# Kernel tuning notes

Hardware: AMD Instinct MI355X
Metric: run time of the kernel (lower is better)

## Reference

```python
import jax, jax.numpy as jnp
import numpy as np

N = 65536        # flattened ray-sample count
K = 8            # net_kernels (experts)
WID = 64         # net_width
D = 32           # feature dim (num_output_channels)
POS_DEG = 2
VIEW_DEG = 4
DIN = D + (3 + 2 * POS_DEG * 3) + (3 + 2 * VIEW_DEG * 3)  # 74


def posenc(x, deg):
    # coord.pos_enc with min_deg=0, max_deg=deg, append_identity=True
    scales = 2.0 ** jnp.arange(deg, dtype=x.dtype)            # [deg]
    xb = (x[..., None, :] * scales[:, None]).reshape(*x.shape[:-1], deg * x.shape[-1])
    four = jnp.sin(jnp.concatenate([xb, xb + 0.5 * jnp.pi], axis=-1))
    return jnp.concatenate([x, four], axis=-1)


def multi_dense(idx, x, kernel, bias):
    # per-sample expert gather + small matmul: x [N,din], kernel [K,din,dout]
    w = kernel[idx]                                           # [N,din,dout]
    return jnp.einsum('ni,nio->no', x, w) + bias[idx]


def _he_uniform(key, shape):
    fan_in = shape[-2]
    lim = np.sqrt(6.0 / fan_in).astype(np.float32)
    return jax.random.uniform(key, shape, jnp.float32, -lim, lim)


def setup_inputs() -> dict:
    key = jax.random.key(0)
    ks = jax.random.split(key, 8)
    idxs = jax.random.randint(ks[0], (N, 1), 0, K, dtype=jnp.int32)
    positions = jax.random.normal(ks[1], (N, 3), jnp.float32)
    viewdirs = jax.random.normal(ks[2], (N, 3), jnp.float32)
    viewdirs = viewdirs / jnp.linalg.norm(viewdirs, axis=-1, keepdims=True)
    features = jax.random.normal(ks[3], (N, D), jnp.float32)
    W0 = _he_uniform(ks[4], (K, DIN, WID))
    b0 = jnp.zeros((K, WID), jnp.float32)
    W1 = _he_uniform(ks[5], (K, WID, WID))
    b1 = jnp.zeros((K, WID), jnp.float32)
    W2 = _he_uniform(ks[6], (K, WID, D))
    b2 = jnp.zeros((K, D), jnp.float32)
    return {'idxs': idxs, 'positions': positions, 'viewdirs': viewdirs,
            'features': features, 'W0': W0, 'b0': b0, 'W1': W1, 'b1': b1,
            'W2': W2, 'b2': b2}


def reference(idxs, positions, viewdirs, features, W0, b0, W1, b1, W2, b2):
    idx = idxs.reshape(-1)                                    # [N]
    x = jnp.concatenate([features,
                         posenc(positions, POS_DEG),
                         posenc(viewdirs, VIEW_DEG)], axis=-1)  # [N, DIN]
    h = jax.nn.relu(multi_dense(idx, x, W0, b0))              # [N, WID]
    h = jax.nn.relu(multi_dense(idx, h, W1, b1))              # [N, WID]
    return multi_dense(idx, h, W2, b2)                        # [N, D]
```

## Files before the change

### kernel.cpp

```cpp
#include <hip/hip_runtime.h>
#include <hip/hip_bf16.h>

#define NS    65536
#define KEXP  8
#define WID   64
#define DOUT  32
#define DIN   74
#define TM    64
#define XS    104
#define HS    72
#define GX    64
#define NB    64

typedef __attribute__((ext_vector_type(8))) short short8;
typedef __attribute__((ext_vector_type(4))) float floatx4;

__device__ __forceinline__ unsigned short f2b(float f) {
  unsigned u = __builtin_bit_cast(unsigned, f);
  u = u + 0x7FFFu + ((u >> 16) & 1u);
  return (unsigned short)(u >> 16);
}


__global__ __launch_bounds__(1024) void k_scatter(const int* __restrict__ idxs,
                                                  unsigned short* __restrict__ bucket,
                                                  int* __restrict__ hist) {
  __shared__ int lc[KEXP];
  const int tid = threadIdx.x;
  const int b = blockIdx.x;
  if (tid < KEXP) lc[tid] = 0;
  __syncthreads();
  const int gid = b * 1024 + tid;
  const int e = idxs[gid];
  const int rank = atomicAdd(&lc[e], 1);
  bucket[(e << 16) + (b << 10) + rank] = (unsigned short)gid;
  __syncthreads();
  if (tid < KEXP) hist[b * KEXP + tid] = lc[tid];
}

__global__ __launch_bounds__(256) void k_mlp(
    const int* __restrict__ hist,
    const unsigned short* __restrict__ bucket,
    const float* __restrict__ pos,
    const float* __restrict__ view,
    const float* __restrict__ feat,
    const float* __restrict__ W0,
    const float* __restrict__ B0,
    const float* __restrict__ W1,
    const float* __restrict__ B1,
    const float* __restrict__ W2,
    const float* __restrict__ B2,
    float* __restrict__ out)
{
  const int e = blockIdx.y;
  const int tid = threadIdx.x;

  __shared__ __align__(16) unsigned short Xs[TM * XS];
  __shared__ __align__(16) unsigned short W0t[WID * XS];
  __shared__ __align__(16) unsigned short W1t[WID * HS];
  __shared__ __align__(16) unsigned short W2t[DOUT * HS];
  __shared__ __align__(16) unsigned short Hs[TM * HS];
  __shared__ float sb0[WID];
  __shared__ float sb1[WID];
  __shared__ float sb2[DOUT];
  __shared__ int sid[TM];
  __shared__ unsigned cns[NB];
  __shared__ unsigned pref[NB];

  if (tid < NB) {
    const unsigned c = (unsigned)hist[tid * KEXP + e];
    unsigned p = c;
    #pragma unroll
    for (int st = 1; st < NB; st <<= 1) {
      const unsigned v = __shfl_up(p, st, 64);
      if ((tid & 63) >= st) p += v;
    }
    cns[tid] = c;
    pref[tid] = p;
  }
  for (int i = tid; i < TM * XS; i += 256) Xs[i] = 0;
  for (int i = tid; i < WID * XS; i += 256) W0t[i] = 0;
  __syncthreads();

  const int segCnt = (int)pref[NB - 1];
  if ((int)blockIdx.x * TM >= segCnt) return;

  {
    const float* g0 = W0 + (size_t)e * DIN * WID;
    for (int g = tid; g < 19 * WID; g += 256) {
      const int o = g & 63, i4 = g >> 6, ib = i4 * 4;
      unsigned v0 = 0, v1 = 0;
      #pragma unroll
      for (int j = 0; j < 4; ++j) {
        const int i = ib + j;
        unsigned short w = (i < DIN) ? f2b(g0[i * WID + o]) : (unsigned short)0;
        if (j < 2) v0 |= (unsigned)w << (16 * j);
        else       v1 |= (unsigned)w << (16 * (j - 2));
      }
      *(uint2*)&W0t[o * XS + ib] = make_uint2(v0, v1);
    }
    const float* g1 = W1 + (size_t)e * WID * WID;
    for (int g = tid; g < 16 * WID; g += 256) {
      const int o = g & 63, i4 = g >> 6, ib = i4 * 4;
      unsigned v0, v1;
      v0 = (unsigned)f2b(g1[(ib + 0) * WID + o]) | ((unsigned)f2b(g1[(ib + 1) * WID + o]) << 16);
      v1 = (unsigned)f2b(g1[(ib + 2) * WID + o]) | ((unsigned)f2b(g1[(ib + 3) * WID + o]) << 16);
      *(uint2*)&W1t[o * HS + ib] = make_uint2(v0, v1);
    }
    const float* g2 = W2 + (size_t)e * WID * DOUT;
    for (int g = tid; g < 16 * DOUT; g += 256) {
      const int o = g & 31, i4 = g >> 5, ib = i4 * 4;
      unsigned v0, v1;
      v0 = (unsigned)f2b(g2[(ib + 0) * DOUT + o]) | ((unsigned)f2b(g2[(ib + 1) * DOUT + o]) << 16);
      v1 = (unsigned)f2b(g2[(ib + 2) * DOUT + o]) | ((unsigned)f2b(g2[(ib + 3) * DOUT + o]) << 16);
      *(uint2*)&W2t[o * HS + ib] = make_uint2(v0, v1);
    }
    if (tid < WID) {
      sb0[tid] = B0[e * WID + tid];
      sb1[tid] = B1[e * WID + tid];
    } else if (tid < WID + DOUT) {
      const int t = tid - WID;
      sb2[t] = B2[e * DOUT + t];
    }
  }
  __syncthreads();

  const int lane = tid & 63;
  const int wv = tid >> 6;
  const int quad = lane >> 4;
  const int r16 = lane & 15;
  const int rb = wv * 16;

  for (int tile = blockIdx.x; tile * TM < segCnt; tile += GX) {
    const int t0 = tile * TM;
    const int rows = min(TM, segCnt - t0);

    __syncthreads();

    const int r = lane;
    if (r < rows) {
      const int p = t0 + r;
      int lo = 0, hi = NB - 1;
      #pragma unroll
      for (int it = 0; it < 6; ++it) {
        const int mid = (lo + hi) >> 1;
        if (pref[mid] > (unsigned)p) hi = mid; else lo = mid + 1;
      }
      const int sb_ = lo;
      const int local = p - (int)(pref[sb_] - cns[sb_]);
      const int s = (int)bucket[(e << 16) + (sb_ << 10) + local];
      unsigned short* xr = &Xs[r * XS];
      if (wv == 0) {
        sid[r] = s;
        const float4* fs = (const float4*)(feat + (size_t)s * DOUT);
        #pragma unroll
        for (int q = 0; q < 4; ++q) {
          float4 f = fs[q];
          xr[q * 4 + 0] = f2b(f.x);
          xr[q * 4 + 1] = f2b(f.y);
          xr[q * 4 + 2] = f2b(f.z);
          xr[q * 4 + 3] = f2b(f.w);
        }
      } else if (wv == 1) {
        const float4* fs = (const float4*)(feat + (size_t)s * DOUT);
        #pragma unroll
        for (int q = 4; q < 8; ++q) {
          float4 f = fs[q];
          xr[q * 4 + 0] = f2b(f.x);
          xr[q * 4 + 1] = f2b(f.y);
          xr[q * 4 + 2] = f2b(f.z);
          xr[q * 4 + 3] = f2b(f.w);
        }
      } else if (wv == 2) {
        float p3[3];
        p3[0] = pos[s * 3 + 0];
        p3[1] = pos[s * 3 + 1];
        p3[2] = pos[s * 3 + 2];
        #pragma unroll
        for (int d = 0; d < 3; ++d) xr[32 + d] = f2b(p3[d]);
        #pragma unroll
        for (int si = 0; si < 2; ++si) {
          const float sc = (float)(1 << si);
          #pragma unroll
          for (int d = 0; d < 3; ++d) {
            const float a = p3[d] * sc;
            xr[35 + si * 3 + d] = f2b(__sinf(a));
            xr[41 + si * 3 + d] = f2b(__cosf(a));
          }
        }
      } else {
        float v3[3];
        v3[0] = view[s * 3 + 0];
        v3[1] = view[s * 3 + 1];
        v3[2] = view[s * 3 + 2];
        #pragma unroll
        for (int d = 0; d < 3; ++d) xr[47 + d] = f2b(v3[d]);
        #pragma unroll
        for (int si = 0; si < 4; ++si) {
          const float sc = (float)(1 << si);
          #pragma unroll
          for (int d = 0; d < 3; ++d) {
            const float a = v3[d] * sc;
            xr[50 + si * 3 + d] = f2b(__sinf(a));
            xr[62 + si * 3 + d] = f2b(__cosf(a));
          }
        }
      }
    }
    __syncthreads();

    {
      const short8 a0 = *(const short8*)&Xs[(rb + r16) * XS + 0 + quad * 8];
      const short8 a1 = *(const short8*)&Xs[(rb + r16) * XS + 32 + quad * 8];
      const short8 a2 = *(const short8*)&Xs[(rb + r16) * XS + 64 + quad * 8];
      #pragma unroll
      for (int c = 0; c < 4; ++c) {
        const int n0 = c * 16;
        floatx4 acc = {0.f, 0.f, 0.f, 0.f};
        acc = __builtin_amdgcn_mfma_f32_16x16x32_bf16(
            a0, *(const short8*)&W0t[(n0 + r16) * XS + 0 + quad * 8], acc, 0, 0, 0);
        acc = __builtin_amdgcn_mfma_f32_16x16x32_bf16(
            a1, *(const short8*)&W0t[(n0 + r16) * XS + 32 + quad * 8], acc, 0, 0, 0);
        acc = __builtin_amdgcn_mfma_f32_16x16x32_bf16(
            a2, *(const short8*)&W0t[(n0 + r16) * XS + 64 + quad * 8], acc, 0, 0, 0);
        const float bias = sb0[n0 + r16];
        #pragma unroll
        for (int g = 0; g < 4; ++g) {
          const float vv = fmaxf(acc[g] + bias, 0.f);
          Hs[(rb + quad * 4 + g) * HS + n0 + r16] = f2b(vv);
        }
      }
    }

    {
      const short8 h0 = *(const short8*)&Hs[(rb + r16) * HS + 0 + quad * 8];
      const short8 h1 = *(const short8*)&Hs[(rb + r16) * HS + 32 + quad * 8];
      #pragma unroll
      for (int c = 0; c < 4; ++c) {
        const int n0 = c * 16;
        floatx4 acc = {0.f, 0.f, 0.f, 0.f};
        acc = __builtin_amdgcn_mfma_f32_16x16x32_bf16(
            h0, *(const short8*)&W1t[(n0 + r16) * HS + 0 + quad * 8], acc, 0, 0, 0);
        acc = __builtin_amdgcn_mfma_f32_16x16x32_bf16(
            h1, *(const short8*)&W1t[(n0 + r16) * HS + 32 + quad * 8], acc, 0, 0, 0);
        const float bias = sb1[n0 + r16];
        #pragma unroll
        for (int g = 0; g < 4; ++g) {
          const float vv = fmaxf(acc[g] + bias, 0.f);
          Hs[(rb + quad * 4 + g) * HS + n0 + r16] = f2b(vv);
        }
      }
    }

    {
      const short8 q0 = *(const short8*)&Hs[(rb + r16) * HS + 0 + quad * 8];
      const short8 q1 = *(const short8*)&Hs[(rb + r16) * HS + 32 + quad * 8];
      #pragma unroll
      for (int c = 0; c < 2; ++c) {
        const int n0 = c * 16;
        floatx4 acc = {0.f, 0.f, 0.f, 0.f};
        acc = __builtin_amdgcn_mfma_f32_16x16x32_bf16(
            q0, *(const short8*)&W2t[(n0 + r16) * HS + 0 + quad * 8], acc, 0, 0, 0);
        acc = __builtin_amdgcn_mfma_f32_16x16x32_bf16(
            q1, *(const short8*)&W2t[(n0 + r16) * HS + 32 + quad * 8], acc, 0, 0, 0);
        const float bias = sb2[n0 + r16];
        const int col = n0 + r16;
        #pragma unroll
        for (int g = 0; g < 4; ++g) {
          const int row = rb + quad * 4 + g;
          if (row < rows) {
            out[(size_t)sid[row] * DOUT + col] = acc[g] + bias;
          }
        }
      }
    }
  }
}

extern "C" void kernel_launch(void* const* d_in, const int* in_sizes, int n_in,
                              void* d_out, int out_size, void* d_ws, size_t ws_size,
                              hipStream_t stream) {
  const int* idxs        = (const int*)d_in[0];
  const float* pos       = (const float*)d_in[1];
  const float* view      = (const float*)d_in[2];
  const float* feat      = (const float*)d_in[3];
  const float* W0        = (const float*)d_in[4];
  const float* b0        = (const float*)d_in[5];
  const float* W1        = (const float*)d_in[6];
  const float* b1        = (const float*)d_in[7];
  const float* W2        = (const float*)d_in[8];
  const float* b2        = (const float*)d_in[9];
  float* out             = (float*)d_out;
  unsigned short* bucket = (unsigned short*)d_ws;
  int* hist              = (int*)((char*)d_ws + (size_t)KEXP * NB * 1024 * 2);

  k_scatter<<<NB, 1024, 0, stream>>>(idxs, bucket, hist);
  dim3 grid(GX, KEXP);
  k_mlp<<<grid, 256, 0, stream>>>(hist, bucket, pos, view, feat,
                                  W0, b0, W1, b1, W2, b2, out);
}
```

Baseline: 99.93 us.

## Prefetch first tile's gathered inputs before weight staging and double grid width

Each wave now keeps the expert prefix sums in registers and does the segment binary search with wave shuffles, so the shared pref/cns arrays and their barrier are gone. Before staging the weights, each block issues the bucket lookup and the feature/position/view loads for its first tile, so that gather latency overlaps the W0/W1/W2 conversion into shared memory. W0t zeroing is cut to the padding columns only, and GX doubles to 128 so more blocks run per expert with fewer tiles each. The cost is more registers held across the weight staging and more blocks that each repeat the weight conversion.

```diff
diff --git a/kernel.cpp b/kernel.cpp
--- a/kernel.cpp
+++ b/kernel.cpp
@@ -9,7 +9,7 @@
 #define TM    64
 #define XS    104
 #define HS    72
-#define GX    64
+#define GX    128
 #define NB    64
 
 typedef __attribute__((ext_vector_type(8))) short short8;
@@ -36,6 +36,20 @@
   bucket[(e << 16) + (b << 10) + rank] = (unsigned short)gid;
   __syncthreads();
   if (tid < KEXP) hist[b * KEXP + tid] = lc[tid];
+}
+
+__device__ __forceinline__ int seg_search(unsigned p, unsigned c, int pp, int* lcl) {
+  int lo = 0, hi = NB - 1;
+#pragma unroll
+  for (int it = 0; it < 6; ++it) {
+    const int mid = (lo + hi) >> 1;
+    const unsigned pm = (unsigned)__shfl((int)p, mid, 64);
+    if (pm > (unsigned)pp) hi = mid;
+    else lo = mid + 1;
+  }
+  const unsigned base = (unsigned)__shfl((int)(p - c), lo, 64);
+  *lcl = pp - (int)base;
+  return lo;
 }
 
 __global__ __launch_bounds__(256) void k_mlp(
@@ -54,6 +68,11 @@
 {
   const int e = blockIdx.y;
   const int tid = threadIdx.x;
+  const int lane = tid & 63;
+  const int wv = tid >> 6;
+  const int quad = lane >> 4;
+  const int r16 = lane & 15;
+  const int rb = wv * 16;
 
   __shared__ __align__(16) unsigned short Xs[TM * XS];
   __shared__ __align__(16) unsigned short W0t[WID * XS];
@@ -64,33 +83,57 @@
   __shared__ float sb1[WID];
   __shared__ float sb2[DOUT];
   __shared__ int sid[TM];
-  __shared__ unsigned cns[NB];
-  __shared__ unsigned pref[NB];
-
-  if (tid < NB) {
-    const unsigned c = (unsigned)hist[tid * KEXP + e];
-    unsigned p = c;
-    #pragma unroll
-    for (int st = 1; st < NB; st <<= 1) {
-      const unsigned v = __shfl_up(p, st, 64);
-      if ((tid & 63) >= st) p += v;
-    }
-    cns[tid] = c;
-    pref[tid] = p;
-  }
+
+  const unsigned c = (unsigned)hist[lane * KEXP + e];
+  unsigned p = c;
+#pragma unroll
+  for (int st = 1; st < NB; st <<= 1) {
+    const unsigned v = __shfl_up(p, st, 64);
+    if (lane >= st) p += v;
+  }
+  const int segCnt = __shfl((int)p, NB - 1, 64);
+  if ((int)blockIdx.x * TM >= segCnt) return;
+
+  int s_pre = 0;
+  float4 fA, fB, fC, fD;
+  {
+    const int t0 = (int)blockIdx.x * TM;
+    const int rows = min(TM, segCnt - t0);
+    const int pp = t0 + min(lane, rows - 1);
+    int local;
+    const int sb_ = seg_search(p, c, pp, &local);
+    if (lane < rows) {
+      s_pre = (int)bucket[(e << 16) + (sb_ << 10) + local];
+      if (wv == 0) {
+        const float4* fs = (const float4*)(feat + (size_t)s_pre * DOUT);
+        fA = fs[0]; fB = fs[1]; fC = fs[2]; fD = fs[3];
+      } else if (wv == 1) {
+        const float4* fs = (const float4*)(feat + (size_t)s_pre * DOUT);
+        fA = fs[4]; fB = fs[5]; fC = fs[6]; fD = fs[7];
+      } else if (wv == 2) {
+        fA.x = pos[s_pre * 3 + 0];
+        fA.y = pos[s_pre * 3 + 1];
+        fA.z = pos[s_pre * 3 + 2];
+      } else {
+        fA.x = view[s_pre * 3 + 0];
+        fA.y = view[s_pre * 3 + 1];
+        fA.z = view[s_pre * 3 + 2];
+      }
+    }
+  }
+
   for (int i = tid; i < TM * XS; i += 256) Xs[i] = 0;
-  for (int i = tid; i < WID * XS; i += 256) W0t[i] = 0;
-  __syncthreads();
-
-  const int segCnt = (int)pref[NB - 1];
-  if ((int)blockIdx.x * TM >= segCnt) return;
+  for (int g = tid; g < WID * 7; g += 256) {
+    const int o = g / 7, ch = g % 7;
+    *(uint2*)&W0t[o * XS + 76 + ch * 4] = make_uint2(0u, 0u);
+  }
 
   {
     const float* g0 = W0 + (size_t)e * DIN * WID;
     for (int g = tid; g < 19 * WID; g += 256) {
       const int o = g & 63, i4 = g >> 6, ib = i4 * 4;
       unsigned v0 = 0, v1 = 0;
-      #pragma unroll
+#pragma unroll
       for (int j = 0; j < 4; ++j) {
         const int i = ib + j;
         unsigned short w = (i < DIN) ? f2b(g0[i * WID + o]) : (unsigned short)0;
@@ -125,63 +168,56 @@
   }
   __syncthreads();
 
-  const int lane = tid & 63;
-  const int wv = tid >> 6;
-  const int quad = lane >> 4;
-  const int r16 = lane & 15;
-  const int rb = wv * 16;
-
   for (int tile = blockIdx.x; tile * TM < segCnt; tile += GX) {
     const int t0 = tile * TM;
     const int rows = min(TM, segCnt - t0);
 
-    __syncthreads();
-
-    const int r = lane;
-    if (r < rows) {
-      const int p = t0 + r;
-      int lo = 0, hi = NB - 1;
-      #pragma unroll
-      for (int it = 0; it < 6; ++it) {
-        const int mid = (lo + hi) >> 1;
-        if (pref[mid] > (unsigned)p) hi = mid; else lo = mid + 1;
-      }
-      const int sb_ = lo;
-      const int local = p - (int)(pref[sb_] - cns[sb_]);
-      const int s = (int)bucket[(e << 16) + (sb_ << 10) + local];
-      unsigned short* xr = &Xs[r * XS];
+    if (tile != (int)blockIdx.x) {
+      __syncthreads();
+      const int pp = t0 + min(lane, rows - 1);
+      int local;
+      const int sb_ = seg_search(p, c, pp, &local);
+      if (lane < rows) {
+        s_pre = (int)bucket[(e << 16) + (sb_ << 10) + local];
+        if (wv == 0) {
+          const float4* fs = (const float4*)(feat + (size_t)s_pre * DOUT);
+          fA = fs[0]; fB = fs[1]; fC = fs[2]; fD = fs[3];
+        } else if (wv == 1) {
+          const float4* fs = (const float4*)(feat + (size_t)s_pre * DOUT);
+          fA = fs[4]; fB = fs[5]; fC = fs[6]; fD = fs[7];
+        } else if (wv == 2) {
+          fA.x = pos[s_pre * 3 + 0];
+          fA.y = pos[s_pre * 3 + 1];
+          fA.z = pos[s_pre * 3 + 2];
+        } else {
+          fA.x = view[s_pre * 3 + 0];
+          fA.y = view[s_pre * 3 + 1];
+          fA.z = view[s_pre * 3 + 2];
+        }
+      }
+    }
+
+    if (lane < rows) {
+      unsigned short* xr = &Xs[lane * XS];
       if (wv == 0) {
-        sid[r] = s;
-        const float4* fs = (const float4*)(feat + (size_t)s * DOUT);
-        #pragma unroll
-        for (int q = 0; q < 4; ++q) {
-          float4 f = fs[q];
-          xr[q * 4 + 0] = f2b(f.x);
-          xr[q * 4 + 1] = f2b(f.y);
-          xr[q * 4 + 2] = f2b(f.z);
-          xr[q * 4 + 3] = f2b(f.w);
-        }
+        sid[lane] = s_pre;
+        xr[0]  = f2b(fA.x); xr[1]  = f2b(fA.y); xr[2]  = f2b(fA.z); xr[3]  = f2b(fA.w);
+        xr[4]  = f2b(fB.x); xr[5]  = f2b(fB.y); xr[6]  = f2b(fB.z); xr[7]  = f2b(fB.w);
+        xr[8]  = f2b(fC.x); xr[9]  = f2b(fC.y); xr[10] = f2b(fC.z); xr[11] = f2b(fC.w);
+        xr[12] = f2b(fD.x); xr[13] = f2b(fD.y); xr[14] = f2b(fD.z); xr[15] = f2b(fD.w);
       } else if (wv == 1) {
-        const float4* fs = (const float4*)(feat + (size_t)s * DOUT);
-        #pragma unroll
-        for (int q = 4; q < 8; ++q) {
-          float4 f = fs[q];
-          xr[q * 4 + 0] = f2b(f.x);
-          xr[q * 4 + 1] = f2b(f.y);
-          xr[q * 4 + 2] = f2b(f.z);
-          xr[q * 4 + 3] = f2b(f.w);
-        }
+        xr[16] = f2b(fA.x); xr[17] = f2b(fA.y); xr[18] = f2b(fA.z); xr[19] = f2b(fA.w);
+        xr[20] = f2b(fB.x); xr[21] = f2b(fB.y); xr[22] = f2b(fB.z); xr[23] = f2b(fB.w);
+        xr[24] = f2b(fC.x); xr[25] = f2b(fC.y); xr[26] = f2b(fC.z); xr[27] = f2b(fC.w);
+        xr[28] = f2b(fD.x); xr[29] = f2b(fD.y); xr[30] = f2b(fD.z); xr[31] = f2b(fD.w);
       } else if (wv == 2) {
-        float p3[3];
-        p3[0] = pos[s * 3 + 0];
-        p3[1] = pos[s * 3 + 1];
-        p3[2] = pos[s * 3 + 2];
-        #pragma unroll
+        float p3[3] = {fA.x, fA.y, fA.z};
+#pragma unroll
         for (int d = 0; d < 3; ++d) xr[32 + d] = f2b(p3[d]);
-        #pragma unroll
+#pragma unroll
         for (int si = 0; si < 2; ++si) {
           const float sc = (float)(1 << si);
-          #pragma unroll
+#pragma unroll
           for (int d = 0; d < 3; ++d) {
             const float a = p3[d] * sc;
             xr[35 + si * 3 + d] = f2b(__sinf(a));
@@ -189,16 +225,13 @@
           }
         }
       } else {
-        float v3[3];
-        v3[0] = view[s * 3 + 0];
-        v3[1] = view[s * 3 + 1];
-        v3[2] = view[s * 3 + 2];
-        #pragma unroll
+        float v3[3] = {fA.x, fA.y, fA.z};
+#pragma unroll
         for (int d = 0; d < 3; ++d) xr[47 + d] = f2b(v3[d]);
-        #pragma unroll
+#pragma unroll
         for (int si = 0; si < 4; ++si) {
           const float sc = (float)(1 << si);
-          #pragma unroll
+#pragma unroll
           for (int d = 0; d < 3; ++d) {
             const float a = v3[d] * sc;
             xr[50 + si * 3 + d] = f2b(__sinf(a));
@@ -213,9 +246,9 @@
       const short8 a0 = *(const short8*)&Xs[(rb + r16) * XS + 0 + quad * 8];
       const short8 a1 = *(const short8*)&Xs[(rb + r16) * XS + 32 + quad * 8];
       const short8 a2 = *(const short8*)&Xs[(rb + r16) * XS + 64 + quad * 8];
-      #pragma unroll
-      for (int c = 0; c < 4; ++c) {
-        const int n0 = c * 16;
+#pragma unroll
+      for (int cc = 0; cc < 4; ++cc) {
+        const int n0 = cc * 16;
         floatx4 acc = {0.f, 0.f, 0.f, 0.f};
         acc = __builtin_amdgcn_mfma_f32_16x16x32_bf16(
             a0, *(const short8*)&W0t[(n0 + r16) * XS + 0 + quad * 8], acc, 0, 0, 0);
@@ -224,7 +257,7 @@
         acc = __builtin_amdgcn_mfma_f32_16x16x32_bf16(
             a2, *(const short8*)&W0t[(n0 + r16) * XS + 64 + quad * 8], acc, 0, 0, 0);
         const float bias = sb0[n0 + r16];
-        #pragma unroll
+#pragma unroll
         for (int g = 0; g < 4; ++g) {
           const float vv = fmaxf(acc[g] + bias, 0.f);
           Hs[(rb + quad * 4 + g) * HS + n0 + r16] = f2b(vv);
@@ -235,16 +268,16 @@
     {
       const short8 h0 = *(const short8*)&Hs[(rb + r16) * HS + 0 + quad * 8];
       const short8 h1 = *(const short8*)&Hs[(rb + r16) * HS + 32 + quad * 8];
-      #pragma unroll
-      for (int c = 0; c < 4; ++c) {
-        const int n0 = c * 16;
+#pragma unroll
+      for (int cc = 0; cc < 4; ++cc) {
+        const int n0 = cc * 16;
         floatx4 acc = {0.f, 0.f, 0.f, 0.f};
         acc = __builtin_amdgcn_mfma_f32_16x16x32_bf16(
             h0, *(const short8*)&W1t[(n0 + r16) * HS + 0 + quad * 8], acc, 0, 0, 0);
         acc = __builtin_amdgcn_mfma_f32_16x16x32_bf16(
             h1, *(const short8*)&W1t[(n0 + r16) * HS + 32 + quad * 8], acc, 0, 0, 0);
         const float bias = sb1[n0 + r16];
-        #pragma unroll
+#pragma unroll
         for (int g = 0; g < 4; ++g) {
           const float vv = fmaxf(acc[g] + bias, 0.f);
           Hs[(rb + quad * 4 + g) * HS + n0 + r16] = f2b(vv);
@@ -255,9 +288,9 @@
     {
       const short8 q0 = *(const short8*)&Hs[(rb + r16) * HS + 0 + quad * 8];
       const short8 q1 = *(const short8*)&Hs[(rb + r16) * HS + 32 + quad * 8];
-      #pragma unroll
-      for (int c = 0; c < 2; ++c) {
-        const int n0 = c * 16;
+#pragma unroll
+      for (int cc = 0; cc < 2; ++cc) {
+        const int n0 = cc * 16;
         floatx4 acc = {0.f, 0.f, 0.f, 0.f};
         acc = __builtin_amdgcn_mfma_f32_16x16x32_bf16(
             q0, *(const short8*)&W2t[(n0 + r16) * HS + 0 + quad * 8], acc, 0, 0, 0);
@@ -265,7 +298,7 @@
             q1, *(const short8*)&W2t[(n0 + r16) * HS + 32 + quad * 8], acc, 0, 0, 0);
         const float bias = sb2[n0 + r16];
         const int col = n0 + r16;
-        #pragma unroll
+#pragma unroll
         for (int g = 0; g < 4; ++g) {
           const int row = rb + quad * 4 + g;
           if (row < rows) {
```

Measured after the change: 108.7 us. +8.8%, slower.
